# Kernel tuning notes

Measured on AMD Instinct MI355X. Metric: run time of the kernel, lower is better.

Reference implementation:

```python
import jax, jax.numpy as jnp
import numpy as np

M_A, N_B, S_A, S_B = 2, 2, 1, 1  # sharing chunks and base strides


def setup_inputs() -> dict:
    key = jax.random.key(0)
    ks = jax.random.split(key, 7)
    B, S, D_IN, D_OUT = 4, 2048, 4096, 4096
    U, SHARED_R = 8, 56  # rank=64, unshared u=8
    x = jax.random.normal(ks[0], (B, S, D_IN), jnp.float32)
    W = jax.random.normal(ks[1], (D_OUT, D_IN), jnp.float32) * 0.02
    b = jax.random.normal(ks[2], (D_OUT,), jnp.float32) * 0.02
    A_u = jax.random.normal(ks[3], (U, D_IN), jnp.float32) * 0.02
    B_u = jax.random.normal(ks[4], (D_OUT, U), jnp.float32) * 0.02
    A0_shared = jax.random.normal(ks[5], (SHARED_R, D_IN // M_A), jnp.float32) * 0.02
    B0_shared = jax.random.normal(ks[6], (D_OUT // N_B, SHARED_R), jnp.float32) * 0.02
    return {"x": x, "W": W, "b": b, "A_u": A_u, "B_u": B_u,
            "A0_shared": A0_shared, "B0_shared": B0_shared}


def reference(x, W, b, A_u, B_u, A0_shared, B0_shared):
    # Rotated shared chunks: roll A0 along rank dim (axis 0), tile along in dim.
    A_s = jnp.concatenate([jnp.roll(A0_shared, i * S_A, axis=0) for i in range(M_A)], axis=1)  # [r_s, in]
    # Roll B0 along rank dim (axis 1), tile along out dim.
    B_s = jnp.concatenate([jnp.roll(B0_shared, i * S_B, axis=1) for i in range(N_B)], axis=0)  # [out, r_s]
    # Full delta_W materialization, as in the original module.
    delta_W = B_u @ A_u + B_s @ A_s  # [out, in]
    original = jnp.einsum('bsd,od->bso', x, W) + b
    adapt = jnp.einsum('bsd,od->bso', x, delta_W)
    return original + adapt
```

## Files before the change

kernel.cpp:

```cpp
#include <hip/hip_runtime.h>

typedef unsigned short u16;
typedef __bf16 bf16x8 __attribute__((ext_vector_type(8)));
typedef float f32x4 __attribute__((ext_vector_type(4)));
typedef u16 u16x8 __attribute__((ext_vector_type(8)));

#define M_DIM 8192
#define N_DIM 4096
#define K_DIM 4096
#define BM 256
#define BN 256
#define BK 64
#define NT (K_DIM / BK)

__device__ __forceinline__ u16 f2b(float f) {
  unsigned int x = __float_as_uint(f);
  unsigned int r = (x + 0x7fffu + ((x >> 16) & 1u)) >> 16;
  return (u16)r;
}

#define GLOAD_LDS16(gp, lp)                                        \
  __builtin_amdgcn_global_load_lds(                                \
      (const __attribute__((address_space(1))) void*)(gp),         \
      (__attribute__((address_space(3))) void*)(lp), 16, 0, 0)

#define BAR __builtin_amdgcn_s_barrier()
#define VMW(N)                                                     \
  do {                                                             \
    asm volatile("s_waitcnt vmcnt(" #N ")" ::: "memory");          \
    __builtin_amdgcn_sched_barrier(0);                             \
  } while (0)

__global__ __launch_bounds__(256) void cvt_x(const float* __restrict__ X,
                                             u16* __restrict__ Xb) {
  const size_t t = (size_t)blockIdx.x * 256 + threadIdx.x;
  const f32x4* src = (const f32x4*)X + t * 2;
  f32x4 a = src[0];
  f32x4 b = src[1];
  u16x8 o;
  o[0] = f2b(a[0]); o[1] = f2b(a[1]); o[2] = f2b(a[2]); o[3] = f2b(a[3]);
  o[4] = f2b(b[0]); o[5] = f2b(b[1]); o[6] = f2b(b[2]); o[7] = f2b(b[3]);
  *((u16x8*)Xb + t) = o;
}

__global__ __launch_bounds__(256) void build_weff(
    const float* __restrict__ W, const float* __restrict__ Au,
    const float* __restrict__ Bu, const float* __restrict__ A0,
    const float* __restrict__ B0, u16* __restrict__ Weff) {
  __shared__ float coef[64 * 16];
  const int t = threadIdx.x;
  const int o0 = blockIdx.y * 16;

#pragma unroll
  for (int j = 0; j < 4; j++) {
    const int idx = t + j * 256;
    const int r = idx >> 4;
    const int oi = idx & 15;
    const int o = o0 + oi;
    float v;
    if (r < 8) {
      v = Bu[o * 8 + r];
    } else {
      const int rs = r - 8;
      if (o < 2048) {
        v = B0[o * 56 + rs];
      } else {
        const int rr = rs ? (rs - 1) : 55;
        v = B0[(o - 2048) * 56 + rr];
      }
    }
    coef[r * 16 + oi] = v;
  }
  __syncthreads();

  const int d0 = blockIdx.x * 1024 + t * 4;
  const int hi = (d0 >= 2048);
  const int dd = hi ? (d0 - 2048) : d0;

  f32x4 acc[16] = {};

#pragma unroll
  for (int r = 0; r < 8; r++) {
    f32x4 a = *(const f32x4*)(Au + (size_t)r * 4096 + d0);
    const float* cr = &coef[r * 16];
#pragma unroll
    for (int oi = 0; oi < 16; oi++) {
      const float c = cr[oi];
      acc[oi][0] += c * a[0]; acc[oi][1] += c * a[1];
      acc[oi][2] += c * a[2]; acc[oi][3] += c * a[3];
    }
  }
#pragma unroll 4
  for (int rs = 0; rs < 56; rs++) {
    const int rr = hi ? (rs ? (rs - 1) : 55) : rs;
    f32x4 a = *(const f32x4*)(A0 + (size_t)rr * 2048 + dd);
    const float* cr = &coef[(rs + 8) * 16];
#pragma unroll
    for (int oi = 0; oi < 16; oi++) {
      const float c = cr[oi];
      acc[oi][0] += c * a[0]; acc[oi][1] += c * a[1];
      acc[oi][2] += c * a[2]; acc[oi][3] += c * a[3];
    }
  }

#pragma unroll
  for (int oi = 0; oi < 16; oi++) {
    f32x4 w = *(const f32x4*)(W + (size_t)(o0 + oi) * 4096 + d0);
    ushort4 ov;
    ov.x = f2b(acc[oi][0] + w[0]);
    ov.y = f2b(acc[oi][1] + w[1]);
    ov.z = f2b(acc[oi][2] + w[2]);
    ov.w = f2b(acc[oi][3] + w[3]);
    *(ushort4*)(Weff + (size_t)(o0 + oi) * 4096 + d0) = ov;
  }
}

__global__ __launch_bounds__(512, 2) void gemm_bt_bias(
    const u16* __restrict__ X, const u16* __restrict__ Wf,
    const float* __restrict__ bias, float* __restrict__ C) {
  __shared__ __align__(16) u16 lds[65536];

  const int tid = threadIdx.x;
  const int wave = tid >> 6;
  const int lane = tid & 63;
  const int wm = wave >> 2;
  const int wn = wave & 3;
  const int quad = lane >> 4;
  const int l16 = lane & 15;

  const int wgid = ((blockIdx.x & 7) << 6) | (blockIdx.x >> 3);
  const int n0 = (wgid & 15) * BN;
  const int m0 = (wgid >> 4) * BM;

  const int srow = lane >> 3;
  const int sq = lane & 7;
  const int scol = ((sq ^ srow) << 3);
  const u16* xg = X + (size_t)(m0 + wave * 8 + srow) * K_DIM + scol;
  const u16* wg = Wf + (size_t)(n0 + wave * 8 + srow) * K_DIM + scol;
  u16* lA = lds + wave * 512;
  u16* lB = lds + 32768 + wave * 512;

#define SG_A(b, r, t)                                                       \
  GLOAD_LDS16(xg + (size_t)(r) * 64 * K_DIM + (size_t)(t) * BK,             \
              lA + (b) * 16384 + (r) * 4096)
#define SG_B(b, r, t)                                                       \
  GLOAD_LDS16(wg + (size_t)(r) * 64 * K_DIM + (size_t)(t) * BK,             \
              lB + (b) * 16384 + (r) * 4096)

  f32x4 acc[8][4] = {};
  bf16x8 afr[4][2];
  bf16x8 bfr[2][2][2];

  const int c0 = (quad << 4) ^ ((l16 & 7) << 4);

#define READ_A(mh, ABASE)                                                   \
  do {                                                                      \
    const char* ab_ =                                                       \
        (ABASE) + (size_t)((wm * 128 + (mh) * 64 + l16) * 128);             \
    _Pragma("unroll") for (int mi = 0; mi < 4; mi++) {                      \
      afr[mi][0] = *(const bf16x8*)(ab_ + mi * 2048 + c0);                  \
      afr[mi][1] = *(const bf16x8*)(ab_ + mi * 2048 + (c0 ^ 64));           \
    }                                                                       \
  } while (0)

#define READ_B(nh, BBASE)                                                   \
  do {                                                                      \
    const char* bb_ =                                                       \
        (BBASE) + (size_t)((wn * 64 + (nh) * 32 + l16) * 128);              \
    _Pragma("unroll") for (int ni = 0; ni < 2; ni++) {                      \
      bfr[nh][ni][0] = *(const bf16x8*)(bb_ + ni * 2048 + c0);              \
      bfr[nh][ni][1] = *(const bf16x8*)(bb_ + ni * 2048 + (c0 ^ 64));       \
    }                                                                       \
  } while (0)

#define MFMA_Q(mh, nh)                                                      \
  do {                                                                      \
    __builtin_amdgcn_s_setprio(1);                                          \
    _Pragma("unroll") for (int mi = 0; mi < 4; mi++) {                      \
      _Pragma("unroll") for (int ni = 0; ni < 2; ni++) {                    \
        acc[(mh)*4 + mi][(nh)*2 + ni] =                                     \
            __builtin_amdgcn_mfma_f32_16x16x32_bf16(                        \
                afr[mi][0], bfr[nh][ni][0],                                 \
                acc[(mh)*4 + mi][(nh)*2 + ni], 0, 0, 0);                    \
        acc[(mh)*4 + mi][(nh)*2 + ni] =                                     \
            __builtin_amdgcn_mfma_f32_16x16x32_bf16(                        \
                afr[mi][1], bfr[nh][ni][1],                                 \
                acc[(mh)*4 + mi][(nh)*2 + ni], 0, 0, 0);                    \
      }                                                                     \
    }                                                                       \
    __builtin_amdgcn_s_setprio(0);                                          \
  } while (0)

  SG_A(0, 0, 0); SG_A(0, 2, 0);
  SG_B(0, 0, 0); SG_B(0, 1, 0);
  SG_B(0, 2, 0); SG_B(0, 3, 0);
  SG_A(0, 1, 0); SG_A(0, 3, 0);
  SG_A(1, 0, 1); SG_A(1, 2, 1);
  VMW(4);
  BAR;
  {
    const char* Ab0 = (const char*)lds;
    const char* Bb0 = (const char*)lds + 65536;
    READ_A(0, Ab0);
    READ_B(0, Bb0);
    READ_B(1, Bb0);
  }

  for (int t = 0; t < NT; ++t) {
    const int buf = t & 1;
    const char* Ab = (const char*)lds + buf * 32768;
    const int t1 = (t + 1 < NT) ? t + 1 : NT - 1;
    const int t2 = (t + 2 < NT) ? t + 2 : NT - 1;
    const int b1 = (t + 1) & 1;
    const int b2 = buf;

    SG_B(b1, 0, t1); SG_B(b1, 1, t1);
    BAR;
    MFMA_Q(0, 0);
    VMW(4);
    BAR;

    SG_B(b1, 2, t1); SG_B(b1, 3, t1);
    BAR;
    MFMA_Q(0, 1);
    READ_A(1, Ab);
    BAR;

    SG_A(b1, 1, t1); SG_A(b1, 3, t1);
    BAR;
    MFMA_Q(1, 1);
    BAR;

    SG_A(b2, 0, t2); SG_A(b2, 2, t2);
    BAR;
    MFMA_Q(1, 0);
    VMW(4);
    BAR;
    {
      const char* AbN = (const char*)lds + b1 * 32768;
      const char* BbN = (const char*)lds + 65536 + b1 * 32768;
      READ_A(0, AbN);
      READ_B(0, BbN);
      READ_B(1, BbN);
    }
  }
  VMW(0);

#pragma unroll
  for (int j = 0; j < 4; j++) {
    const int col = n0 + wn * 64 + j * 16 + l16;
    const float bv = bias[col];
#pragma unroll
    for (int i = 0; i < 8; i++) {
      const int row = m0 + wm * 128 + i * 16 + quad * 4;
#pragma unroll
      for (int r = 0; r < 4; r++) {
        C[(size_t)(row + r) * N_DIM + col] = acc[i][j][r] + bv;
      }
    }
  }
}

extern "C" void kernel_launch(void* const* d_in, const int* in_sizes, int n_in,
                              void* d_out, int out_size, void* d_ws, size_t ws_size,
                              hipStream_t stream) {
  const float* x  = (const float*)d_in[0];
  const float* W  = (const float*)d_in[1];
  const float* b  = (const float*)d_in[2];
  const float* Au = (const float*)d_in[3];
  const float* Bu = (const float*)d_in[4];
  const float* A0 = (const float*)d_in[5];
  const float* B0 = (const float*)d_in[6];
  float* out = (float*)d_out;

  u16* Xb   = (u16*)d_ws;
  u16* Weff = (u16*)((char*)d_ws + (size_t)64 * 1024 * 1024);

  cvt_x<<<16384, 256, 0, stream>>>(x, Xb);
  build_weff<<<dim3(4, 256), 256, 0, stream>>>(W, Au, Bu, A0, B0, Weff);
  gemm_bt_bias<<<dim3(512), dim3(512), 0, stream>>>(Xb, Weff, b, out);
}
```

Before: 551.0 us.

## Double-buffer register fragments to overlap LDS reads with MFMA quadrants

Splits the A and B register fragments into two ping-pong sets so each LDS fragment read is issued alongside the MFMA quadrant that uses the other set. This is meant to hide LDS read latency behind matrix math. The per-iteration schedule is also restructured: global-to-LDS loads are regrouped, there are fewer barriers per K step, and the vmcnt waits change. The cost is more live VGPRs, which may raise register pressure, and a subtler hazard ordering between the LDS buffer reuse and the barriers.

```diff
diff --git a/kernel.cpp b/kernel.cpp
--- a/kernel.cpp
+++ b/kernel.cpp
@@ -140,109 +140,99 @@
   u16* lA = lds + wave * 512;
   u16* lB = lds + 32768 + wave * 512;
 
-#define SG_A(b, r, t)                                                       \
-  GLOAD_LDS16(xg + (size_t)(r) * 64 * K_DIM + (size_t)(t) * BK,             \
+#define SG_A(b, r, kt)                                                      \
+  GLOAD_LDS16(xg + (size_t)(r) * 64 * K_DIM + (size_t)(kt) * BK,            \
               lA + (b) * 16384 + (r) * 4096)
-#define SG_B(b, r, t)                                                       \
-  GLOAD_LDS16(wg + (size_t)(r) * 64 * K_DIM + (size_t)(t) * BK,             \
+#define SG_B(b, r, kt)                                                      \
+  GLOAD_LDS16(wg + (size_t)(r) * 64 * K_DIM + (size_t)(kt) * BK,            \
               lB + (b) * 16384 + (r) * 4096)
 
   f32x4 acc[8][4] = {};
-  bf16x8 afr[4][2];
-  bf16x8 bfr[2][2][2];
+  bf16x8 afr0[4][2];
+  bf16x8 afr1[4][2];
+  bf16x8 bfr0[2][2];
+  bf16x8 bfr1[2][2];
 
   const int c0 = (quad << 4) ^ ((l16 & 7) << 4);
 
-#define READ_A(mh, ABASE)                                                   \
+#define READ_A(dst, mh, ABASE)                                              \
   do {                                                                      \
     const char* ab_ =                                                       \
         (ABASE) + (size_t)((wm * 128 + (mh) * 64 + l16) * 128);             \
     _Pragma("unroll") for (int mi = 0; mi < 4; mi++) {                      \
-      afr[mi][0] = *(const bf16x8*)(ab_ + mi * 2048 + c0);                  \
-      afr[mi][1] = *(const bf16x8*)(ab_ + mi * 2048 + (c0 ^ 64));           \
+      dst[mi][0] = *(const bf16x8*)(ab_ + mi * 2048 + c0);                  \
+      dst[mi][1] = *(const bf16x8*)(ab_ + mi * 2048 + (c0 ^ 64));           \
     }                                                                       \
   } while (0)
 
-#define READ_B(nh, BBASE)                                                   \
+#define READ_B(dst, nh, BBASE)                                              \
   do {                                                                      \
     const char* bb_ =                                                       \
         (BBASE) + (size_t)((wn * 64 + (nh) * 32 + l16) * 128);              \
     _Pragma("unroll") for (int ni = 0; ni < 2; ni++) {                      \
-      bfr[nh][ni][0] = *(const bf16x8*)(bb_ + ni * 2048 + c0);              \
-      bfr[nh][ni][1] = *(const bf16x8*)(bb_ + ni * 2048 + (c0 ^ 64));       \
+      dst[ni][0] = *(const bf16x8*)(bb_ + ni * 2048 + c0);                  \
+      dst[ni][1] = *(const bf16x8*)(bb_ + ni * 2048 + (c0 ^ 64));           \
     }                                                                       \
   } while (0)
 
-#define MFMA_Q(mh, nh)                                                      \
+#define MFMA_Q(mh, nh, AF, BF)                                              \
   do {                                                                      \
     __builtin_amdgcn_s_setprio(1);                                          \
     _Pragma("unroll") for (int mi = 0; mi < 4; mi++) {                      \
       _Pragma("unroll") for (int ni = 0; ni < 2; ni++) {                    \
         acc[(mh)*4 + mi][(nh)*2 + ni] =                                     \
             __builtin_amdgcn_mfma_f32_16x16x32_bf16(                        \
-                afr[mi][0], bfr[nh][ni][0],                                 \
+                AF[mi][0], BF[ni][0],                                       \
                 acc[(mh)*4 + mi][(nh)*2 + ni], 0, 0, 0);                    \
         acc[(mh)*4 + mi][(nh)*2 + ni] =                                     \
             __builtin_amdgcn_mfma_f32_16x16x32_bf16(                        \
-                afr[mi][1], bfr[nh][ni][1],                                 \
+                AF[mi][1], BF[ni][1],                                       \
                 acc[(mh)*4 + mi][(nh)*2 + ni], 0, 0, 0);                    \
       }                                                                     \
     }                                                                       \
     __builtin_amdgcn_s_setprio(0);                                          \
   } while (0)
 
+  SG_B(0, 0, 0); SG_B(0, 1, 0); SG_B(0, 2, 0); SG_B(0, 3, 0);
   SG_A(0, 0, 0); SG_A(0, 2, 0);
-  SG_B(0, 0, 0); SG_B(0, 1, 0);
-  SG_B(0, 2, 0); SG_B(0, 3, 0);
   SG_A(0, 1, 0); SG_A(0, 3, 0);
   SG_A(1, 0, 1); SG_A(1, 2, 1);
   VMW(4);
   BAR;
-  {
-    const char* Ab0 = (const char*)lds;
-    const char* Bb0 = (const char*)lds + 65536;
-    READ_A(0, Ab0);
-    READ_B(0, Bb0);
-    READ_B(1, Bb0);
-  }
-
-  for (int t = 0; t < NT; ++t) {
-    const int buf = t & 1;
+  READ_A(afr0, 0, (const char*)lds);
+  READ_B(bfr0, 0, (const char*)lds + 65536);
+
+  for (int T = 0; T < NT; ++T) {
+    const int buf = T & 1;
+    const int b1 = buf ^ 1;
     const char* Ab = (const char*)lds + buf * 32768;
-    const int t1 = (t + 1 < NT) ? t + 1 : NT - 1;
-    const int t2 = (t + 2 < NT) ? t + 2 : NT - 1;
-    const int b1 = (t + 1) & 1;
-    const int b2 = buf;
-
-    SG_B(b1, 0, t1); SG_B(b1, 1, t1);
-    BAR;
-    MFMA_Q(0, 0);
+    const char* AbN = (const char*)lds + b1 * 32768;
+    const char* Bb = (const char*)lds + 65536 + buf * 32768;
+    const char* BbN = (const char*)lds + 65536 + b1 * 32768;
+    const int k1 = (T + 1 < NT) ? T + 1 : NT - 1;
+    const int k2 = (T + 2 < NT) ? T + 2 : NT - 1;
+
+    SG_B(b1, 0, k1); SG_B(b1, 1, k1); SG_B(b1, 2, k1); SG_B(b1, 3, k1);
+    READ_B(bfr1, 1, Bb);
+    MFMA_Q(0, 0, afr0, bfr0);
+    VMW(6);
+    BAR;
+
+    SG_A(b1, 1, k1); SG_A(b1, 3, k1);
+    READ_A(afr1, 1, Ab);
+    MFMA_Q(0, 1, afr0, bfr1);
+    VMW(6);
+    BAR;
+
+    SG_A(buf, 0, k2); SG_A(buf, 2, k2);
+    READ_A(afr0, 0, AbN);
+    MFMA_Q(1, 0, afr1, bfr0);
     VMW(4);
     BAR;
 
-    SG_B(b1, 2, t1); SG_B(b1, 3, t1);
-    BAR;
-    MFMA_Q(0, 1);
-    READ_A(1, Ab);
-    BAR;
-
-    SG_A(b1, 1, t1); SG_A(b1, 3, t1);
-    BAR;
-    MFMA_Q(1, 1);
-    BAR;
-
-    SG_A(b2, 0, t2); SG_A(b2, 2, t2);
-    BAR;
-    MFMA_Q(1, 0);
-    VMW(4);
-    BAR;
-    {
-      const char* AbN = (const char*)lds + b1 * 32768;
-      const char* BbN = (const char*)lds + 65536 + b1 * 32768;
-      READ_A(0, AbN);
-      READ_B(0, BbN);
-      READ_B(1, BbN);
-    }
+    READ_B(bfr0, 0, BbN);
+    MFMA_Q(1, 1, afr1, bfr1);
+    BAR;
   }
   VMW(0);
 
```

New measurement: 540.2 us. 2.0% less time.
